# Kernel tuning notes

Hardware: AMD Instinct MI355X
Metric: run time of the kernel (lower is better)

Reference implementation:

```python
import jax, jax.numpy as jnp
import numpy as np

NUM_FEATURE = 50


def setup_inputs() -> dict:
    key = jax.random.key(0)
    k1, = jax.random.split(key, 1)
    T = 500000
    query = jax.random.normal(k1, (T, NUM_FEATURE), dtype=jnp.float32)
    # Learned params exactly as the torch module initializes them:
    # ql.weight filled with 1 (shape [1, 50] -> we keep [50]), qW scalar 1.0
    ql_w = jnp.ones((NUM_FEATURE,), dtype=jnp.float32)
    qW = jnp.asarray(1.0, dtype=jnp.float32)
    return {"query": query, "ql_w": ql_w, "qW": qW}


def reference(query, ql_w, qW):
    # scores[i] = ql(tanh(qW * query[i]))  -> [T]
    scores = jnp.tanh(qW * query) @ ql_w
    # alpha = softmax(scores) over the T dimension (stable, single pass)
    alpha = jax.nn.softmax(scores, axis=0)
    # z = sum_i alpha[i] * query[i]  -> [NUM_FEATURE]
    z = alpha @ query
    return z
```

## Files before the change

kernel.cpp:

```cpp
#include <hip/hip_runtime.h>
#include <math.h>

#define NF 50
#define REC 52
#define NBLK 1024
#define GRP_PER_BLK 32
#define LOG2E 1.44269504f

__device__ __forceinline__ float row16_allsum(float v) {
    float t;
    t = __int_as_float(__builtin_amdgcn_update_dpp(0, __float_as_int(v), 0x121, 0xF, 0xF, true)); v += t;
    t = __int_as_float(__builtin_amdgcn_update_dpp(0, __float_as_int(v), 0x122, 0xF, 0xF, true)); v += t;
    t = __int_as_float(__builtin_amdgcn_update_dpp(0, __float_as_int(v), 0x124, 0xF, 0xF, true)); v += t;
    t = __int_as_float(__builtin_amdgcn_update_dpp(0, __float_as_int(v), 0x128, 0xF, 0xF, true)); v += t;
    return v;
}

__device__ __forceinline__ float row_partial(float2 a, float2 b, float c2,
                                             float wA0, float wA1, float wB0, float wB1) {
    float r0 = __builtin_amdgcn_rcpf(__builtin_amdgcn_exp2f(c2 * a.x) + 1.f);
    float r1 = __builtin_amdgcn_rcpf(__builtin_amdgcn_exp2f(c2 * a.y) + 1.f);
    float r2 = __builtin_amdgcn_rcpf(__builtin_amdgcn_exp2f(c2 * b.x) + 1.f);
    float r3 = __builtin_amdgcn_rcpf(__builtin_amdgcn_exp2f(c2 * b.y) + 1.f);
    return fmaf(wA0, r0, fmaf(wA1, r1, fmaf(wB0, r2, wB1 * r3)));
}

__global__ __launch_bounds__(512, 8) void attn_pass1(
    const float* __restrict__ query, const float* __restrict__ ql_w,
    const float* __restrict__ qWp, float* __restrict__ ws,
    int T, int totalGroups)
{
    const float qW = qWp[0];
    const int tid  = threadIdx.x;
    const int j    = tid & 15;
    const int gIn  = tid >> 4;
    const int gGlob = blockIdx.x * GRP_PER_BLK + gIn;

    float wA0 = 0.f, wA1 = 0.f, wB0 = 0.f, wB1 = 0.f;
    if (j < 13) { wA0 = ql_w[2*j];     wA1 = ql_w[2*j+1]; }
    if (j < 12) { wB0 = ql_w[26+2*j];  wB1 = ql_w[27+2*j]; }

    const float sumAbsW = row16_allsum(fabsf(wA0)+fabsf(wA1)+fabsf(wB0)+fabsf(wB1));
    const float sumW    = row16_allsum(wA0 + wA1 + wB0 + wB1);
    const float M0 = (sumAbsW > 80.f) ? (sumAbsW - 80.f) : 0.f;
    const float c2 = 2.f * qW * LOG2E;
    const float K  = (sumW - M0) * LOG2E;
    const float n2l = -2.f * LOG2E;

    float s = 0.f, z0 = 0.f, z1 = 0.f, z2 = 0.f, z3 = 0.f;

    const int stride = totalGroups;
    int row = gGlob;
    for (; row + 3*stride < T; row += 4*stride) {
        const float2* q0 = (const float2*)(query + (size_t)row * NF);
        const float2* q1 = (const float2*)(query + (size_t)(row +   stride) * NF);
        const float2* q2 = (const float2*)(query + (size_t)(row + 2*stride) * NF);
        const float2* q3 = (const float2*)(query + (size_t)(row + 3*stride) * NF);
        float2 a0 = make_float2(0.f,0.f), b0 = make_float2(0.f,0.f);
        float2 a1 = make_float2(0.f,0.f), b1 = make_float2(0.f,0.f);
        float2 a2 = make_float2(0.f,0.f), b2 = make_float2(0.f,0.f);
        float2 a3 = make_float2(0.f,0.f), b3 = make_float2(0.f,0.f);
        if (j < 13) { a0 = q0[j];    a1 = q1[j];    a2 = q2[j];    a3 = q3[j]; }
        if (j < 12) { b0 = q0[13+j]; b1 = q1[13+j]; b2 = q2[13+j]; b3 = q3[13+j]; }

        float p0 = row_partial(a0, b0, c2, wA0, wA1, wB0, wB1);
        float p1 = row_partial(a1, b1, c2, wA0, wA1, wB0, wB1);
        float p2 = row_partial(a2, b2, c2, wA0, wA1, wB0, wB1);
        float p3 = row_partial(a3, b3, c2, wA0, wA1, wB0, wB1);
        p0 = row16_allsum(p0);
        p1 = row16_allsum(p1);
        p2 = row16_allsum(p2);
        p3 = row16_allsum(p3);
        float e0 = __builtin_amdgcn_exp2f(fmaf(p0, n2l, K));
        float e1 = __builtin_amdgcn_exp2f(fmaf(p1, n2l, K));
        float e2 = __builtin_amdgcn_exp2f(fmaf(p2, n2l, K));
        float e3 = __builtin_amdgcn_exp2f(fmaf(p3, n2l, K));

        s += (e0 + e1) + (e2 + e3);
        z0 = fmaf(e0, a0.x, fmaf(e1, a1.x, fmaf(e2, a2.x, fmaf(e3, a3.x, z0))));
        z1 = fmaf(e0, a0.y, fmaf(e1, a1.y, fmaf(e2, a2.y, fmaf(e3, a3.y, z1))));
        z2 = fmaf(e0, b0.x, fmaf(e1, b1.x, fmaf(e2, b2.x, fmaf(e3, b3.x, z2))));
        z3 = fmaf(e0, b0.y, fmaf(e1, b1.y, fmaf(e2, b2.y, fmaf(e3, b3.y, z3))));
    }
    for (; row < T; row += stride) {
        const float2* q0 = (const float2*)(query + (size_t)row * NF);
        float2 a = make_float2(0.f,0.f), b = make_float2(0.f,0.f);
        if (j < 13) a = q0[j];
        if (j < 12) b = q0[13+j];
        float p = row_partial(a, b, c2, wA0, wA1, wB0, wB1);
        p = row16_allsum(p);
        float e = __builtin_amdgcn_exp2f(fmaf(p, n2l, K));
        s += e;
        z0 = fmaf(e, a.x, z0);
        z1 = fmaf(e, a.y, z1);
        z2 = fmaf(e, b.x, z2);
        z3 = fmaf(e, b.y, z3);
    }

    __shared__ float sz[GRP_PER_BLK][REC];
    if (j < 13) { sz[gIn][2*j]    = z0; sz[gIn][2*j+1]  = z1; }
    if (j < 12) { sz[gIn][26+2*j] = z2; sz[gIn][27+2*j] = z3; }
    if (j == 13) { sz[gIn][50] = s; sz[gIn][51] = 0.f; }
    __syncthreads();

    if (tid < 51) {
        float acc = 0.f;
        #pragma unroll
        for (int h = 0; h < GRP_PER_BLK; ++h) acc += sz[h][tid];
        ws[(size_t)blockIdx.x * REC + tid] = acc;
    }
}

__global__ __launch_bounds__(1024) void attn_pass2(
    const float* __restrict__ ws, float* __restrict__ out, int B)
{
    __shared__ float zacc[16][REC];
    const int tid = threadIdx.x;
    const int w = tid >> 6, lane = tid & 63;

    if (lane < 51) {
        float acc = 0.f;
        int b = w;
        for (; b + 112 < B; b += 128) {
            acc += ws[(size_t)(b      ) * REC + lane]
                 + ws[(size_t)(b +  16) * REC + lane]
                 + ws[(size_t)(b +  32) * REC + lane]
                 + ws[(size_t)(b +  48) * REC + lane]
                 + ws[(size_t)(b +  64) * REC + lane]
                 + ws[(size_t)(b +  80) * REC + lane]
                 + ws[(size_t)(b +  96) * REC + lane]
                 + ws[(size_t)(b + 112) * REC + lane];
        }
        for (; b < B; b += 16)
            acc += ws[(size_t)b * REC + lane];
        zacc[w][lane] = acc;
    }
    __syncthreads();
    if (tid < NF) {
        float Z = 0.f, S = 0.f;
        #pragma unroll
        for (int h = 0; h < 16; ++h) { Z += zacc[h][tid]; S += zacc[h][50]; }
        out[tid] = Z / S;
    }
}

extern "C" void kernel_launch(void* const* d_in, const int* in_sizes, int n_in,
                              void* d_out, int out_size, void* d_ws, size_t ws_size,
                              hipStream_t stream) {
    const float* query = (const float*)d_in[0];
    const float* ql_w  = (const float*)d_in[1];
    const float* qW    = (const float*)d_in[2];
    float* out = (float*)d_out;
    float* ws  = (float*)d_ws;

    const int T = in_sizes[0] / NF;

    int B = NBLK;
    size_t need = (size_t)B * REC * sizeof(float);
    if (ws_size < need) {
        B = (int)(ws_size / (REC * sizeof(float)));
        if (B < 1) B = 1;
    }

    const int totalGroups = B * GRP_PER_BLK;
    hipLaunchKernelGGL(attn_pass1, dim3(B), dim3(512), 0, stream,
                       query, ql_w, qW, ws, T, totalGroups);
    hipLaunchKernelGGL(attn_pass2, dim3(1), dim3(1024), 0, stream,
                       ws, out, B);
}
```

Before: 28.37 us.

## Process each row with 4 lanes instead of 16 and defer cross-lane reduction

```diff
diff --git a/kernel.cpp b/kernel.cpp
--- a/kernel.cpp
+++ b/kernel.cpp
@@ -3,110 +3,133 @@
 
 #define NF 50
 #define REC 52
-#define NBLK 1024
-#define GRP_PER_BLK 32
+#define NBLK 512
 #define LOG2E 1.44269504f
 
-__device__ __forceinline__ float row16_allsum(float v) {
+#define DPP_QXOR1 0xB1
+#define DPP_QXOR2 0x4E
+#define DPP_ROR4  0x124
+#define DPP_ROR8  0x128
+
+__device__ __forceinline__ float dpp_add(float v, int ctrl) {
     float t;
-    t = __int_as_float(__builtin_amdgcn_update_dpp(0, __float_as_int(v), 0x121, 0xF, 0xF, true)); v += t;
-    t = __int_as_float(__builtin_amdgcn_update_dpp(0, __float_as_int(v), 0x122, 0xF, 0xF, true)); v += t;
-    t = __int_as_float(__builtin_amdgcn_update_dpp(0, __float_as_int(v), 0x124, 0xF, 0xF, true)); v += t;
-    t = __int_as_float(__builtin_amdgcn_update_dpp(0, __float_as_int(v), 0x128, 0xF, 0xF, true)); v += t;
-    return v;
+    switch (ctrl) {
+      case DPP_QXOR1: t = __int_as_float(__builtin_amdgcn_update_dpp(0, __float_as_int(v), DPP_QXOR1, 0xF, 0xF, true)); break;
+      case DPP_QXOR2: t = __int_as_float(__builtin_amdgcn_update_dpp(0, __float_as_int(v), DPP_QXOR2, 0xF, 0xF, true)); break;
+      case DPP_ROR4:  t = __int_as_float(__builtin_amdgcn_update_dpp(0, __float_as_int(v), DPP_ROR4,  0xF, 0xF, true)); break;
+      default:        t = __int_as_float(__builtin_amdgcn_update_dpp(0, __float_as_int(v), DPP_ROR8,  0xF, 0xF, true)); break;
+    }
+    return v + t;
 }
 
-__device__ __forceinline__ float row_partial(float2 a, float2 b, float c2,
-                                             float wA0, float wA1, float wB0, float wB1) {
-    float r0 = __builtin_amdgcn_rcpf(__builtin_amdgcn_exp2f(c2 * a.x) + 1.f);
-    float r1 = __builtin_amdgcn_rcpf(__builtin_amdgcn_exp2f(c2 * a.y) + 1.f);
-    float r2 = __builtin_amdgcn_rcpf(__builtin_amdgcn_exp2f(c2 * b.x) + 1.f);
-    float r3 = __builtin_amdgcn_rcpf(__builtin_amdgcn_exp2f(c2 * b.y) + 1.f);
-    return fmaf(wA0, r0, fmaf(wA1, r1, fmaf(wB0, r2, wB1 * r3)));
-}
-
-__global__ __launch_bounds__(512, 8) void attn_pass1(
+__global__ __launch_bounds__(512, 4) void attn_pass1(
     const float* __restrict__ query, const float* __restrict__ ql_w,
     const float* __restrict__ qWp, float* __restrict__ ws,
     int T, int totalGroups)
 {
     const float qW = qWp[0];
-    const int tid  = threadIdx.x;
-    const int j    = tid & 15;
-    const int gIn  = tid >> 4;
-    const int gGlob = blockIdx.x * GRP_PER_BLK + gIn;
+    const int tid = threadIdx.x;
+    const int q   = tid & 3;
+    const int g   = blockIdx.x * 128 + (tid >> 2);
 
-    float wA0 = 0.f, wA1 = 0.f, wB0 = 0.f, wB1 = 0.f;
-    if (j < 13) { wA0 = ql_w[2*j];     wA1 = ql_w[2*j+1]; }
-    if (j < 12) { wB0 = ql_w[26+2*j];  wB1 = ql_w[27+2*j]; }
+    float2 w01[7];
+    #pragma unroll
+    for (int t = 0; t < 6; ++t) {
+        const int s = q + 4 * t;
+        w01[t] = *(const float2*)(ql_w + 2 * s);
+    }
+    w01[6] = (q == 0) ? *(const float2*)(ql_w + 48) : make_float2(0.f, 0.f);
+    const int d6 = (q == 0) ? 192 : 160;
 
-    const float sumAbsW = row16_allsum(fabsf(wA0)+fabsf(wA1)+fabsf(wB0)+fabsf(wB1));
-    const float sumW    = row16_allsum(wA0 + wA1 + wB0 + wB1);
-    const float M0 = (sumAbsW > 80.f) ? (sumAbsW - 80.f) : 0.f;
-    const float c2 = 2.f * qW * LOG2E;
-    const float K  = (sumW - M0) * LOG2E;
+    float sw = 0.f, saw = 0.f;
+    #pragma unroll
+    for (int t = 0; t < 7; ++t) {
+        sw  += w01[t].x + w01[t].y;
+        saw += fabsf(w01[t].x) + fabsf(w01[t].y);
+    }
+    sw  = dpp_add(dpp_add(sw,  DPP_QXOR1), DPP_QXOR2);
+    saw = dpp_add(dpp_add(saw, DPP_QXOR1), DPP_QXOR2);
+    const float M0  = (saw > 80.f) ? (saw - 80.f) : 0.f;
+    const float c2  = 2.f * qW * LOG2E;
+    const float K   = (sw - M0) * LOG2E;
     const float n2l = -2.f * LOG2E;
 
-    float s = 0.f, z0 = 0.f, z1 = 0.f, z2 = 0.f, z3 = 0.f;
+    float2 z[7];
+    #pragma unroll
+    for (int t = 0; t < 7; ++t) z[t] = make_float2(0.f, 0.f);
+    float se = 0.f;
 
-    const int stride = totalGroups;
-    int row = gGlob;
-    for (; row + 3*stride < T; row += 4*stride) {
-        const float2* q0 = (const float2*)(query + (size_t)row * NF);
-        const float2* q1 = (const float2*)(query + (size_t)(row +   stride) * NF);
-        const float2* q2 = (const float2*)(query + (size_t)(row + 2*stride) * NF);
-        const float2* q3 = (const float2*)(query + (size_t)(row + 3*stride) * NF);
-        float2 a0 = make_float2(0.f,0.f), b0 = make_float2(0.f,0.f);
-        float2 a1 = make_float2(0.f,0.f), b1 = make_float2(0.f,0.f);
-        float2 a2 = make_float2(0.f,0.f), b2 = make_float2(0.f,0.f);
-        float2 a3 = make_float2(0.f,0.f), b3 = make_float2(0.f,0.f);
-        if (j < 13) { a0 = q0[j];    a1 = q1[j];    a2 = q2[j];    a3 = q3[j]; }
-        if (j < 12) { b0 = q0[13+j]; b1 = q1[13+j]; b2 = q2[13+j]; b3 = q3[13+j]; }
+    const int G = totalGroups;
+    const char* rp = (const char*)(query + (size_t)g * NF) + (q << 3);
+    const size_t step = (size_t)G * NF * sizeof(float);
 
-        float p0 = row_partial(a0, b0, c2, wA0, wA1, wB0, wB1);
-        float p1 = row_partial(a1, b1, c2, wA0, wA1, wB0, wB1);
-        float p2 = row_partial(a2, b2, c2, wA0, wA1, wB0, wB1);
-        float p3 = row_partial(a3, b3, c2, wA0, wA1, wB0, wB1);
-        p0 = row16_allsum(p0);
-        p1 = row16_allsum(p1);
-        p2 = row16_allsum(p2);
-        p3 = row16_allsum(p3);
-        float e0 = __builtin_amdgcn_exp2f(fmaf(p0, n2l, K));
-        float e1 = __builtin_amdgcn_exp2f(fmaf(p1, n2l, K));
-        float e2 = __builtin_amdgcn_exp2f(fmaf(p2, n2l, K));
-        float e3 = __builtin_amdgcn_exp2f(fmaf(p3, n2l, K));
+    for (int row = g; row < T; row += G, rp += step) {
+        float2 x0 = *(const float2*)(rp);
+        float2 x1 = *(const float2*)(rp + 32);
+        float2 x2 = *(const float2*)(rp + 64);
+        float2 x3 = *(const float2*)(rp + 96);
+        float2 x4 = *(const float2*)(rp + 128);
+        float2 x5 = *(const float2*)(rp + 160);
+        float2 x6 = *(const float2*)(rp + d6);
 
-        s += (e0 + e1) + (e2 + e3);
-        z0 = fmaf(e0, a0.x, fmaf(e1, a1.x, fmaf(e2, a2.x, fmaf(e3, a3.x, z0))));
-        z1 = fmaf(e0, a0.y, fmaf(e1, a1.y, fmaf(e2, a2.y, fmaf(e3, a3.y, z1))));
-        z2 = fmaf(e0, b0.x, fmaf(e1, b1.x, fmaf(e2, b2.x, fmaf(e3, b3.x, z2))));
-        z3 = fmaf(e0, b0.y, fmaf(e1, b1.y, fmaf(e2, b2.y, fmaf(e3, b3.y, z3))));
-    }
-    for (; row < T; row += stride) {
-        const float2* q0 = (const float2*)(query + (size_t)row * NF);
-        float2 a = make_float2(0.f,0.f), b = make_float2(0.f,0.f);
-        if (j < 13) a = q0[j];
-        if (j < 12) b = q0[13+j];
-        float p = row_partial(a, b, c2, wA0, wA1, wB0, wB1);
-        p = row16_allsum(p);
-        float e = __builtin_amdgcn_exp2f(fmaf(p, n2l, K));
-        s += e;
-        z0 = fmaf(e, a.x, z0);
-        z1 = fmaf(e, a.y, z1);
-        z2 = fmaf(e, b.x, z2);
-        z3 = fmaf(e, b.y, z3);
+        float p = 0.f;
+        {
+            float r;
+            r = __builtin_amdgcn_rcpf(__builtin_amdgcn_exp2f(c2 * x0.x) + 1.f); p = fmaf(w01[0].x, r, p);
+            r = __builtin_amdgcn_rcpf(__builtin_amdgcn_exp2f(c2 * x0.y) + 1.f); p = fmaf(w01[0].y, r, p);
+            r = __builtin_amdgcn_rcpf(__builtin_amdgcn_exp2f(c2 * x1.x) + 1.f); p = fmaf(w01[1].x, r, p);
+            r = __builtin_amdgcn_rcpf(__builtin_amdgcn_exp2f(c2 * x1.y) + 1.f); p = fmaf(w01[1].y, r, p);
+            r = __builtin_amdgcn_rcpf(__builtin_amdgcn_exp2f(c2 * x2.x) + 1.f); p = fmaf(w01[2].x, r, p);
+            r = __builtin_amdgcn_rcpf(__builtin_amdgcn_exp2f(c2 * x2.y) + 1.f); p = fmaf(w01[2].y, r, p);
+            r = __builtin_amdgcn_rcpf(__builtin_amdgcn_exp2f(c2 * x3.x) + 1.f); p = fmaf(w01[3].x, r, p);
+            r = __builtin_amdgcn_rcpf(__builtin_amdgcn_exp2f(c2 * x3.y) + 1.f); p = fmaf(w01[3].y, r, p);
+            r = __builtin_amdgcn_rcpf(__builtin_amdgcn_exp2f(c2 * x4.x) + 1.f); p = fmaf(w01[4].x, r, p);
+            r = __builtin_amdgcn_rcpf(__builtin_amdgcn_exp2f(c2 * x4.y) + 1.f); p = fmaf(w01[4].y, r, p);
+            r = __builtin_amdgcn_rcpf(__builtin_amdgcn_exp2f(c2 * x5.x) + 1.f); p = fmaf(w01[5].x, r, p);
+            r = __builtin_amdgcn_rcpf(__builtin_amdgcn_exp2f(c2 * x5.y) + 1.f); p = fmaf(w01[5].y, r, p);
+            r = __builtin_amdgcn_rcpf(__builtin_amdgcn_exp2f(c2 * x6.x) + 1.f); p = fmaf(w01[6].x, r, p);
+            r = __builtin_amdgcn_rcpf(__builtin_amdgcn_exp2f(c2 * x6.y) + 1.f); p = fmaf(w01[6].y, r, p);
+        }
+        p = dpp_add(dpp_add(p, DPP_QXOR1), DPP_QXOR2);
+        const float e = __builtin_amdgcn_exp2f(fmaf(p, n2l, K));
+
+        se += e;
+        z[0].x = fmaf(e, x0.x, z[0].x); z[0].y = fmaf(e, x0.y, z[0].y);
+        z[1].x = fmaf(e, x1.x, z[1].x); z[1].y = fmaf(e, x1.y, z[1].y);
+        z[2].x = fmaf(e, x2.x, z[2].x); z[2].y = fmaf(e, x2.y, z[2].y);
+        z[3].x = fmaf(e, x3.x, z[3].x); z[3].y = fmaf(e, x3.y, z[3].y);
+        z[4].x = fmaf(e, x4.x, z[4].x); z[4].y = fmaf(e, x4.y, z[4].y);
+        z[5].x = fmaf(e, x5.x, z[5].x); z[5].y = fmaf(e, x5.y, z[5].y);
+        z[6].x = fmaf(e, x6.x, z[6].x); z[6].y = fmaf(e, x6.y, z[6].y);
     }
 
-    __shared__ float sz[GRP_PER_BLK][REC];
-    if (j < 13) { sz[gIn][2*j]    = z0; sz[gIn][2*j+1]  = z1; }
-    if (j < 12) { sz[gIn][26+2*j] = z2; sz[gIn][27+2*j] = z3; }
-    if (j == 13) { sz[gIn][50] = s; sz[gIn][51] = 0.f; }
+    #pragma unroll
+    for (int t = 0; t < 7; ++t) {
+        z[t].x = dpp_add(dpp_add(z[t].x, DPP_ROR4), DPP_ROR8);
+        z[t].y = dpp_add(dpp_add(z[t].y, DPP_ROR4), DPP_ROR8);
+    }
+    se = dpp_add(dpp_add(se, DPP_ROR4), DPP_ROR8);
+
+    __shared__ float sz[32][REC];
+    if ((tid & 15) < 4) {
+        const int eidx = tid >> 4;
+        #pragma unroll
+        for (int t = 0; t < 6; ++t) {
+            const int s = q + 4 * t;
+            *(float2*)&sz[eidx][2 * s] = z[t];
+        }
+        if (q == 0) {
+            *(float2*)&sz[eidx][48] = z[6];
+            sz[eidx][50] = se;
+            sz[eidx][51] = 0.f;
+        }
+    }
     __syncthreads();
 
     if (tid < 51) {
         float acc = 0.f;
         #pragma unroll
-        for (int h = 0; h < GRP_PER_BLK; ++h) acc += sz[h][tid];
+        for (int h = 0; h < 32; ++h) acc += sz[h][tid];
         ws[(size_t)blockIdx.x * REC + tid] = acc;
     }
 }
@@ -162,7 +185,7 @@
         if (B < 1) B = 1;
     }
 
-    const int totalGroups = B * GRP_PER_BLK;
+    const int totalGroups = B * 128;
     hipLaunchKernelGGL(attn_pass1, dim3(B), dim3(512), 0, stream,
                        query, ql_w, qW, ws, T, totalGroups);
     hipLaunchKernelGGL(attn_pass2, dim3(1), dim3(1024), 0, stream,
```

New measurement: 25.71 us. 9.4% less time.
